# Kernel tuning notes

Measured on AMD Instinct MI355X. Metric: run time of the kernel, lower is better.

## Reference

```python
import jax, jax.numpy as jnp
import numpy as np

B, ORDER, N, D, H = 16, 2, 512, 128, 8
DH = D // H
NEG_SLOPE = 0.2


def setup_inputs() -> dict:
    key = jax.random.key(0)
    ks = jax.random.split(key, 8)
    stdv = 1.0 / np.sqrt(DH)

    def u(k, shape):
        return jax.random.uniform(k, shape, jnp.float32, -stdv, stdv)

    x = jax.random.normal(ks[0], (B, ORDER, N, D), jnp.float32)
    A = jax.random.randint(ks[1], (B, ORDER, N, N), 0, 5, jnp.int32)
    # Stacked params for the 2*order GAT modules: axis0 = order, axis1 = (conv1, conv2)
    W = u(ks[2], (ORDER, 2, D, D))            # project.weight
    pb = jnp.zeros((ORDER, 2, D), jnp.float32)  # project.bias (init 0)
    att_src = u(ks[3], (ORDER, 2, H, DH))
    att_dst = u(ks[4], (ORDER, 2, H, DH))
    bias = jnp.zeros((ORDER, 2, D), jnp.float32)  # GAT output bias (init 0)
    return {"x": x, "A": A, "W": W, "pb": pb,
            "att_src": att_src, "att_dst": att_dst, "bias": bias}


def _gat(x, Af, W, pb, a_src, a_dst, b):
    # x: [B,N,D]; Af: [B,N,N] float in {0,1}
    xp = x @ W.T + pb                                  # project
    xh = xp.reshape(B, N, H, DH)                       # [B,N,H,DH]
    s_src = jnp.einsum('bnhd,hd->bnh', xh, a_src)      # [B,N,H]
    s_dst = jnp.einsum('bnhd,hd->bnh', xh, a_dst)
    alpha = s_src[:, :, None, :] + s_dst[:, None, :, :]  # [B,src,dst,H]
    alpha = jnp.where((Af != 1.0)[..., None], 0.0, alpha)
    alpha = jnp.where(alpha >= 0, alpha, NEG_SLOPE * alpha)  # leaky relu
    alpha = jax.nn.softmax(alpha, axis=1)              # softmax over src dim
    out = jnp.einsum('bsdh,bshf->bdhf', alpha, xh).reshape(B, N, D)
    out = out + xp                                     # add_self_loops
    return out + b


def reference(x, A, W, pb, att_src, att_dst, bias):
    A1 = ((A == 2) | (A == 4)).astype(x.dtype)  # [B,ORDER,N,N]
    A2 = ((A == 3) | (A == 4)).astype(x.dtype)
    hs = []
    for i in range(ORDER):
        h1 = _gat(x[:, i], A1[:, i], W[i, 0], pb[i, 0], att_src[i, 0], att_dst[i, 0], bias[i, 0])
        h2 = _gat(x[:, i], A2[:, i], W[i, 1], pb[i, 1], att_src[i, 1], att_dst[i, 1], bias[i, 1])
        hs.append(h1 + h2)
    h = jnp.stack(hs, axis=1)                          # [B,ORDER,N,D]
    out = h + h.mean(axis=1, keepdims=True)
    return out
```

## Files before the change

### kernel.cpp

```cpp
#include <hip/hip_runtime.h>

#define N_ 512
#define D_ 128
#define LOG2E 1.44269504088896f


typedef __attribute__((ext_vector_type(8))) short short8;
typedef __attribute__((ext_vector_type(4))) float floatx4;
typedef __attribute__((ext_vector_type(4))) unsigned int uintx4;
typedef __attribute__((ext_vector_type(2))) _Float16 half2v;
typedef __attribute__((ext_vector_type(8))) _Float16 half8;

#if defined(__has_builtin)
#if __has_builtin(__builtin_amdgcn_exp2f)
#define EXP2F(x) __builtin_amdgcn_exp2f(x)
#else
#define EXP2F(x) exp2f(x)
#endif
#else
#define EXP2F(x) exp2f(x)
#endif

__device__ __forceinline__ unsigned int pkh(float a, float b) {
    auto h = __builtin_amdgcn_cvt_pkrtz(a, b);
    return __builtin_bit_cast(unsigned int, h);
}

__global__ __launch_bounds__(256) void prep_kernel(
    const float* __restrict__ x, const float* __restrict__ W,
    const float* __restrict__ pb, const float* __restrict__ att_src,
    const float* __restrict__ att_dst, const int* __restrict__ A,
    unsigned short* __restrict__ xpt, unsigned int* __restrict__ sgEs,
    unsigned int* __restrict__ sgFs, float2* __restrict__ sgD,
    unsigned int* __restrict__ mgT)
{
    __shared__ _Float16 va_l[8][136];
    __shared__ float c0_l[8];

    const int bid0 = blockIdx.x;
    const int t = threadIdx.x;

    if (bid0 >= 1024) {
        const int bid = bid0 - 1024;
        const int bi = bid >> 4;
        const int rem = bid & 15;
        const int dg = rem >> 2;
        const int jw = rem & 3;
        const int dp = t & 63, q = t >> 6;
        const int dstb = dg * 128 + dp * 2;
        const int sbase = jw * 128 + q * 8;
        const int* Ab = A + (size_t)bi * N_ * N_ + dstb;
        unsigned int a00 = 0, a01 = 0, a10 = 0, a11 = 0;
#pragma unroll
        for (int cp = 0; cp < 4; ++cp) {
#pragma unroll
            for (int i = 0; i < 8; ++i) {
                const int s = sbase + cp * 32 + i;
                const int2 v = *(const int2*)(Ab + (size_t)s * N_);
                const int bitp = cp * 8 + i;
                a00 |= ((0x14u >> v.x) & 1u) << bitp;
                a10 |= ((0x18u >> v.x) & 1u) << bitp;
                a01 |= ((0x14u >> v.y) & 1u) << bitp;
                a11 |= ((0x18u >> v.y) & 1u) << bitp;
            }
        }
        const int i0 = bi * 2;
        mgT[(((size_t)i0 * 4 + q) * 512 + dstb + 0) * 4 + jw] = a00;
        mgT[(((size_t)i0 * 4 + q) * 512 + dstb + 1) * 4 + jw] = a01;
        mgT[(((size_t)(i0 + 1) * 4 + q) * 512 + dstb + 0) * 4 + jw] = a10;
        mgT[(((size_t)(i0 + 1) * 4 + q) * 512 + dstb + 1) * 4 + jw] = a11;
        return;
    }

    const int unit = bid0 >> 1;
    const int half = bid0 & 1;
    const int ntile = unit & 7;
    const int inst  = unit >> 3;
    const int j = inst & 1;
    const int bi = inst >> 1;
    const int ij = (bi & 1) * 2 + j;
    const int wave = t >> 6, L = t & 63, n = L & 15, q = L >> 4;
    const float* wb = W + (size_t)ij * D_ * D_;

    {
        const int c = t >> 5;
        const int k0 = (t & 31) * 4;
        const int hn = half * 4 + (c & 3);
        const float* av = ((c < 4) ? att_src : att_dst) + ij * D_ + hn * 16;
        const float* Wh = wb + (size_t)(hn * 16) * D_ + k0;
        float a0 = 0.f, a1 = 0.f, a2 = 0.f, a3 = 0.f;
#pragma unroll
        for (int dd = 0; dd < 16; ++dd) {
            const float a = av[dd];
            const float4 wv = *(const float4*)(Wh + (size_t)dd * D_);
            a0 += wv.x * a; a1 += wv.y * a; a2 += wv.z * a; a3 += wv.w * a;
        }
        va_l[c][k0 + 0] = (_Float16)(a0 * LOG2E);
        va_l[c][k0 + 1] = (_Float16)(a1 * LOG2E);
        va_l[c][k0 + 2] = (_Float16)(a2 * LOG2E);
        va_l[c][k0 + 3] = (_Float16)(a3 * LOG2E);
        if (t < 8) {
            const int hn2 = half * 4 + (t & 3);
            const float* av2 = ((t < 4) ? att_src : att_dst) + ij * D_ + hn2 * 16;
            const float* pbp = pb + ij * D_ + hn2 * 16;
            float s = 0.f;
#pragma unroll
            for (int dd = 0; dd < 16; ++dd) s += pbp[dd] * av2[dd];
            c0_l[t] = s * LOG2E;
        }
    }

    const int n0w = ntile * 64 + wave * 16;
    const float* xrow = x + ((size_t)bi * N_ + n0w + n) * D_ + q * 8;
    half8 Af[4];
#pragma unroll
    for (int kc = 0; kc < 4; ++kc) {
        const float4 a0 = *(const float4*)(xrow + kc * 32);
        const float4 a1 = *(const float4*)(xrow + kc * 32 + 4);
        uintx4 au;
        au.x = pkh(a0.x, a0.y);
        au.y = pkh(a0.z, a0.w);
        au.z = pkh(a1.x, a1.y);
        au.w = pkh(a1.z, a1.w);
        Af[kc] = __builtin_bit_cast(half8, au);
    }

    __syncthreads();

    floatx4 S = (floatx4){0.f, 0.f, 0.f, 0.f};
    {
        const _Float16* var = &va_l[n & 7][q * 8];
#pragma unroll
        for (int kc = 0; kc < 4; ++kc) {
            const half8 Bs = *(const half8*)(var + kc * 32);
            S = __builtin_amdgcn_mfma_f32_16x16x32_f16(Af[kc], Bs, S, 0, 0, 0);
        }
    }

#pragma unroll
    for (int ft = 0; ft < 4; ++ft) {
        const int head = half * 4 + ft;
        const int fg = head * 16 + n;
        const float* wrow = wb + (size_t)fg * D_ + q * 8;
        floatx4 C = (floatx4){0.f, 0.f, 0.f, 0.f};
#pragma unroll
        for (int kc = 0; kc < 4; ++kc) {
            const float4 b0 = *(const float4*)(wrow + kc * 32);
            const float4 b1 = *(const float4*)(wrow + kc * 32 + 4);
            uintx4 bu;
            bu.x = pkh(b0.x, b0.y);
            bu.y = pkh(b0.z, b0.w);
            bu.z = pkh(b1.x, b1.y);
            bu.w = pkh(b1.z, b1.w);
            C = __builtin_amdgcn_mfma_f32_16x16x32_f16(
                Af[kc], __builtin_bit_cast(half8, bu), C, 0, 0, 0);
        }
        const float pbv = pb[ij * D_ + fg];
        uint2 pk;
        pk.x = pkh(C[0] + pbv, C[1] + pbv);
        pk.y = pkh(C[2] + pbv, C[3] + pbv);
        *(uint2*)&xpt[((size_t)inst * D_ + fg) * N_ + n0w + q * 4] = pk;
    }

    if (n < 8) {
        const float cc = c0_l[n];
        const float v0 = S[0] + cc, v1 = S[1] + cc;
        const float v2 = S[2] + cc, v3 = S[3] + cc;
        if (n < 4) {
            const int head = half * 4 + n;
            const size_t base = ((size_t)inst * 8 + head) * 256 + (n0w >> 1) + q * 2;
            sgEs[base + 0] = pkh(EXP2F(v0), EXP2F(v1));
            sgEs[base + 1] = pkh(EXP2F(v2), EXP2F(v3));
            sgFs[base + 0] = pkh(EXP2F(0.2f * v0), EXP2F(0.2f * v1));
            sgFs[base + 1] = pkh(EXP2F(0.2f * v2), EXP2F(0.2f * v3));
        } else {
            const int head = half * 4 + (n - 4);
            const size_t base = ((size_t)inst * 8 + head) * N_ + n0w + q * 4;
            float2 e0; e0.x = EXP2F(v0); e0.y = EXP2F(0.2f * v0); sgD[base + 0] = e0;
            float2 e1; e1.x = EXP2F(v1); e1.y = EXP2F(0.2f * v1); sgD[base + 1] = e1;
            float2 e2; e2.x = EXP2F(v2); e2.y = EXP2F(0.2f * v2); sgD[base + 2] = e2;
            float2 e3; e3.x = EXP2F(v3); e3.y = EXP2F(0.2f * v3); sgD[base + 3] = e3;
        }
    }
}

__global__ __launch_bounds__(512, 8) void attn_kernel(
    const unsigned short* __restrict__ xpt,
    const unsigned int* __restrict__ sgEs,
    const unsigned int* __restrict__ sgFs,
    const float2* __restrict__ sgD,
    const unsigned int* __restrict__ mgT,
    const float* __restrict__ bias,
    float* __restrict__ hout)
{
    __shared__ unsigned int smem[8192];
    __shared__ unsigned int seltab[4];

    const int bid = blockIdx.x;
    const int tile = bid & 31;
    const int bi   = bid >> 5;
    const int i0   = bi * 2;
    const int d0 = tile * 16;
    const int t = threadIdx.x;
    const int wave = t >> 6, L = t & 63, n = L & 15, q = L >> 4;
    const int cv = wave >> 2;
    const int h0 = (wave & 3) * 2;
    const int inst = i0 + cv;
    const int ij = (bi & 1) * 2 + cv;

    {
        const uint4* sE = (const uint4*)(sgEs + (size_t)i0 * 2048);
        const uint4* sF = (const uint4*)(sgFs + (size_t)i0 * 2048);
        uint4* dE = (uint4*)smem;
        uint4* dF = (uint4*)(smem + 4096);
        dE[t] = sE[t]; dE[512 + t] = sE[512 + t];
        dF[t] = sF[t]; dF[512 + t] = sF[512 + t];
    }
    if (t < 4) seltab[t] = ((t & 1) ? 0x0000FFFFu : 0u) | ((t & 2) ? 0xFFFF0000u : 0u);

    const uint4 mreg = *(const uint4*)(mgT + (((size_t)inst * 4 + q) * 512 + d0 + n) * 4);
    const unsigned int mw_[4] = { mreg.x, mreg.y, mreg.z, mreg.w };

    unsigned int iEd2[2], rd2[2];
#pragma unroll
    for (int hh = 0; hh < 2; ++hh) {
        const float2 ed = sgD[((size_t)inst * 8 + h0 + hh) * N_ + d0 + n];
        const float iEd = 1.0f / ed.x;
        const float rdv = ed.y * iEd;
        iEd2[hh] = pkh(iEd, iEd);
        rd2[hh] = pkh(rdv, rdv);
    }

    __syncthreads();

    const unsigned short* xpi = xpt + (size_t)inst * D_ * N_;
    const unsigned short* bp0 = xpi + (size_t)(h0 * 16 + n) * N_;
    const unsigned short* bp1 = xpi + (size_t)((h0 + 1) * 16 + n) * N_;
    const unsigned int* esw = smem + cv * 2048;
    const unsigned int* fsw = smem + 4096 + cv * 2048;

    const uintx4 ou = { 0x3C003C00u, 0x3C003C00u, 0x3C003C00u, 0x3C003C00u };
    const half8 onesB = __builtin_bit_cast(half8, ou);

    floatx4 Cacc[2] = { (floatx4){0.f,0.f,0.f,0.f}, (floatx4){0.f,0.f,0.f,0.f} };
    floatx4 Cz[2]   = { (floatx4){0.f,0.f,0.f,0.f}, (floatx4){0.f,0.f,0.f,0.f} };

    uintx4 B0 = *(const uintx4*)(bp0 + q * 8);
    uintx4 B1 = *(const uintx4*)(bp1 + q * 8);
#pragma unroll
    for (int c = 0; c < 16; ++c) {
        const int sq = c * 32 + q * 8;
        uintx4 nB0, nB1;
        if (c < 15) {
            nB0 = *(const uintx4*)(bp0 + sq + 32);
            nB1 = *(const uintx4*)(bp1 + sq + 32);
        }
        const unsigned int word = mw_[c >> 2];
        unsigned int sel[4];
#pragma unroll
        for (int p = 0; p < 4; ++p) {
            const int sh = (c & 3) * 8 + 2 * p;
            const unsigned int b4 = (sh >= 2) ? ((word >> (sh - 2)) & 12u)
                                              : ((word << 2) & 12u);
            sel[p] = *(const unsigned int*)((const char*)seltab + b4);
        }
        const int spb = c * 16 + q * 4;
#pragma unroll
        for (int hh = 0; hh < 2; ++hh) {
            const uint4 Ep = *(const uint4*)&esw[(h0 + hh) * 256 + spb];
            const uint4 Fp = *(const uint4*)&fsw[(h0 + hh) * 256 + spb];
            const unsigned int eu[4] = { Ep.x, Ep.y, Ep.z, Ep.w };
            const unsigned int fu[4] = { Fp.x, Fp.y, Fp.z, Fp.w };
            const half2v rdh = __builtin_bit_cast(half2v, rd2[hh]);
            uintx4 au;
            unsigned int wts[4];
#pragma unroll
            for (int p = 0; p < 4; ++p) {
                const half2v e = __builtin_bit_cast(half2v, eu[p]);
                const half2v f = __builtin_bit_cast(half2v, fu[p]);
                const half2v pr = f * rdh;
                const half2v wv = __builtin_elementwise_max(pr, e);
                const unsigned int wvu = __builtin_bit_cast(unsigned int, wv);
                wts[p] = (sel[p] & wvu) | (~sel[p] & iEd2[hh]);
            }
            au.x = wts[0]; au.y = wts[1]; au.z = wts[2]; au.w = wts[3];
            const half8 As = __builtin_bit_cast(half8, au);
            Cacc[hh] = __builtin_amdgcn_mfma_f32_16x16x32_f16(
                As, __builtin_bit_cast(half8, hh ? B1 : B0), Cacc[hh], 0, 0, 0);
            Cz[hh] = __builtin_amdgcn_mfma_f32_16x16x32_f16(
                As, onesB, Cz[hh], 0, 0, 0);
        }
        B0 = nB0;
        B1 = nB1;
    }

    float vals[2][4];
#pragma unroll
    for (int hh = 0; hh < 2; ++hh) {
        const int h = h0 + hh;
        const float bv = bias[ij * D_ + h * 16 + n];
        const uint2 sv = *(const uint2*)(xpi + (size_t)(h * 16 + n) * N_ + d0 + q * 4);
        const half2v s0 = __builtin_bit_cast(half2v, sv.x);
        const half2v s1 = __builtin_bit_cast(half2v, sv.y);
        const float selfv[4] = { (float)s0[0], (float)s0[1],
                                 (float)s1[0], (float)s1[1] };
#pragma unroll
        for (int reg = 0; reg < 4; ++reg) {
            const float Zi = 1.0f / Cz[hh][reg];
            vals[hh][reg] = Cacc[hh][reg] * Zi + selfv[reg] + bv;
        }
    }

    __syncthreads();
    float* out_l = (float*)smem;
    if (cv == 1) {
#pragma unroll
        for (int hh = 0; hh < 2; ++hh)
#pragma unroll
            for (int reg = 0; reg < 4; ++reg)
                out_l[(q * 4 + reg) * 132 + (h0 + hh) * 16 + n] = vals[hh][reg];
    }
    __syncthreads();
    if (cv == 0) {
#pragma unroll
        for (int hh = 0; hh < 2; ++hh)
#pragma unroll
            for (int reg = 0; reg < 4; ++reg)
                hout[((size_t)bi * N_ + d0 + q * 4 + reg) * D_ + (h0 + hh) * 16 + n] =
                    vals[hh][reg] + out_l[(q * 4 + reg) * 132 + (h0 + hh) * 16 + n];
    }
}

__global__ __launch_bounds__(256) void combine_kernel(float* __restrict__ h)
{
    const int idx = blockIdx.x * 256 + threadIdx.x;
    const int b = idx >> 14;
    const int r = idx & 16383;
    float4* p0 = (float4*)h + (size_t)b * 32768 + r;
    float4* p1 = p0 + 16384;
    const float4 a = *p0;
    const float4 o = *p1;
    float4 r0, r1;
    r0.x = 1.5f * a.x + 0.5f * o.x;  r1.x = 1.5f * o.x + 0.5f * a.x;
    r0.y = 1.5f * a.y + 0.5f * o.y;  r1.y = 1.5f * o.y + 0.5f * a.y;
    r0.z = 1.5f * a.z + 0.5f * o.z;  r1.z = 1.5f * o.z + 0.5f * a.z;
    r0.w = 1.5f * a.w + 0.5f * o.w;  r1.w = 1.5f * o.w + 0.5f * a.w;
    *p0 = r0;
    *p1 = r1;
}

extern "C" void kernel_launch(void* const* d_in, const int* in_sizes, int n_in,
                              void* d_out, int out_size, void* d_ws, size_t ws_size,
                              hipStream_t stream)
{
    const float* x   = (const float*)d_in[0];
    const int*   A   = (const int*)d_in[1];
    const float* W   = (const float*)d_in[2];
    const float* pb  = (const float*)d_in[3];
    const float* as_ = (const float*)d_in[4];
    const float* ad_ = (const float*)d_in[5];
    const float* bs  = (const float*)d_in[6];

    unsigned short* xpt = (unsigned short*)d_ws;
    unsigned int* sgEs = (unsigned int*)((char*)d_ws + (8u << 20));
    unsigned int* sgFs = (unsigned int*)((char*)d_ws + (8u << 20) + (512u << 10));
    float2* sgD = (float2*)((char*)d_ws + (9u << 20));
    unsigned int* mgT = (unsigned int*)((char*)d_ws + (11u << 20));
    float* h = (float*)d_out;

    prep_kernel<<<1536, 256, 0, stream>>>(x, W, pb, as_, ad_, A, xpt, sgEs, sgFs, sgD, mgT);
    attn_kernel<<<1024, 512, 0, stream>>>(xpt, sgEs, sgFs, sgD, mgT, bs, h);
    combine_kernel<<<1024, 256, 0, stream>>>(h);
}
```

Baseline: 153.0 us.

## Remap blocks per XCD, prefetch two chunks ahead, compute masks in registers

Block indices are remapped so that consecutive blocks landing on the same XCD share a batch instance, which is meant to improve L2 reuse of the per-instance inputs. The B-operand prefetch now runs two iterations ahead instead of one, to hide more global-load latency, at the cost of extra registers. The shared-memory lookup table for the half-word select masks is replaced by bit tests computed in registers, which removes LDS reads and one shared array.

```diff
diff --git a/kernel.cpp b/kernel.cpp
--- a/kernel.cpp
+++ b/kernel.cpp
@@ -194,11 +194,12 @@
     float* __restrict__ hout)
 {
     __shared__ unsigned int smem[8192];
-    __shared__ unsigned int seltab[4];
 
     const int bid = blockIdx.x;
-    const int tile = bid & 31;
-    const int bi   = bid >> 5;
+    const int xcd = bid & 7;
+    const int idx = bid >> 3;
+    const int bi  = xcd * 4 + (idx >> 5);
+    const int tile = idx & 31;
     const int i0   = bi * 2;
     const int d0 = tile * 16;
     const int t = threadIdx.x;
@@ -216,7 +217,6 @@
         dE[t] = sE[t]; dE[512 + t] = sE[512 + t];
         dF[t] = sF[t]; dF[512 + t] = sF[512 + t];
     }
-    if (t < 4) seltab[t] = ((t & 1) ? 0x0000FFFFu : 0u) | ((t & 2) ? 0xFFFF0000u : 0u);
 
     const uint4 mreg = *(const uint4*)(mgT + (((size_t)inst * 4 + q) * 512 + d0 + n) * 4);
     const unsigned int mw_[4] = { mreg.x, mreg.y, mreg.z, mreg.w };
@@ -245,24 +245,25 @@
     floatx4 Cacc[2] = { (floatx4){0.f,0.f,0.f,0.f}, (floatx4){0.f,0.f,0.f,0.f} };
     floatx4 Cz[2]   = { (floatx4){0.f,0.f,0.f,0.f}, (floatx4){0.f,0.f,0.f,0.f} };
 
-    uintx4 B0 = *(const uintx4*)(bp0 + q * 8);
-    uintx4 B1 = *(const uintx4*)(bp1 + q * 8);
+    uintx4 A0 = *(const uintx4*)(bp0 + q * 8);
+    uintx4 A1 = *(const uintx4*)(bp1 + q * 8);
+    uintx4 P0 = *(const uintx4*)(bp0 + 32 + q * 8);
+    uintx4 P1 = *(const uintx4*)(bp1 + 32 + q * 8);
 #pragma unroll
     for (int c = 0; c < 16; ++c) {
-        const int sq = c * 32 + q * 8;
-        uintx4 nB0, nB1;
-        if (c < 15) {
-            nB0 = *(const uintx4*)(bp0 + sq + 32);
-            nB1 = *(const uintx4*)(bp1 + sq + 32);
+        uintx4 F0, F1;
+        if (c < 14) {
+            F0 = *(const uintx4*)(bp0 + (c + 2) * 32 + q * 8);
+            F1 = *(const uintx4*)(bp1 + (c + 2) * 32 + q * 8);
         }
         const unsigned int word = mw_[c >> 2];
         unsigned int sel[4];
 #pragma unroll
         for (int p = 0; p < 4; ++p) {
             const int sh = (c & 3) * 8 + 2 * p;
-            const unsigned int b4 = (sh >= 2) ? ((word >> (sh - 2)) & 12u)
-                                              : ((word << 2) & 12u);
-            sel[p] = *(const unsigned int*)((const char*)seltab + b4);
+            const unsigned int wb2 = word >> sh;
+            sel[p] = ((wb2 & 1u) ? 0x0000FFFFu : 0u) |
+                     ((wb2 & 2u) ? 0xFFFF0000u : 0u);
         }
         const int spb = c * 16 + q * 4;
 #pragma unroll
@@ -286,12 +287,12 @@
             au.x = wts[0]; au.y = wts[1]; au.z = wts[2]; au.w = wts[3];
             const half8 As = __builtin_bit_cast(half8, au);
             Cacc[hh] = __builtin_amdgcn_mfma_f32_16x16x32_f16(
-                As, __builtin_bit_cast(half8, hh ? B1 : B0), Cacc[hh], 0, 0, 0);
+                As, __builtin_bit_cast(half8, hh ? A1 : A0), Cacc[hh], 0, 0, 0);
             Cz[hh] = __builtin_amdgcn_mfma_f32_16x16x32_f16(
                 As, onesB, Cz[hh], 0, 0, 0);
         }
-        B0 = nB0;
-        B1 = nB1;
+        A0 = P0; A1 = P1;
+        P0 = F0; P1 = F1;
     }
 
     float vals[2][4];
```

Measured after the change: 150.6 us. About the same (-1.6%).
